# Kernel optimization log

Hardware: AMD Instinct MI355X
Metric: run time of the kernel (lower is better)

## Reference

```python
import math
import jax, jax.numpy as jnp
import numpy as np

B, L = 2, 4096
D_MODEL, D_STATE, D_CONV, EXPAND = 1024, 64, 4, 2
D_INNER = EXPAND * D_MODEL
DT_RANK = max(1, D_MODEL // 16)
EPS = float(jnp.finfo(jnp.float32).eps)  # torch nn.RMSNorm default eps


def setup_inputs() -> dict:
    key = jax.random.key(0)
    ks = jax.random.split(key, 8)
    sc = lambda k, shape, scale: jax.random.normal(k, shape, jnp.float32) * scale
    x = jax.random.normal(ks[0], (B, L, D_MODEL), jnp.float32)
    in_proj_w = sc(ks[1], (2 * D_INNER, D_MODEL), D_MODEL ** -0.5)
    conv_w = sc(ks[2], (D_INNER, 1, D_CONV), D_CONV ** -0.5)  # depthwise kernel
    conv_b = jnp.zeros((D_INNER,), jnp.float32)
    norm_w = jnp.ones((D_INNER,), jnp.float32)
    dt_std = DT_RANK ** -0.5
    dt_w = jax.random.uniform(ks[3], (D_INNER, D_INNER), jnp.float32, -dt_std, dt_std)
    dt_b = jnp.full((D_INNER,), math.log(0.5), jnp.float32)
    A_log = jnp.log(jnp.tile(jnp.arange(1, D_STATE + 1, dtype=jnp.float32), (D_INNER, 1)))
    D = jnp.ones((D_INNER,), jnp.float32)
    B_w = sc(ks[4], (D_STATE, D_INNER), D_INNER ** -0.5)
    C_w = sc(ks[5], (D_STATE, D_INNER), D_INNER ** -0.5)
    out_w = sc(ks[6], (D_MODEL, D_INNER), D_INNER ** -0.5)
    return dict(x=x, in_proj_w=in_proj_w, conv_w=conv_w, conv_b=conv_b,
                norm_w=norm_w, dt_w=dt_w, dt_b=dt_b, A_log=A_log, D=D,
                B_w=B_w, C_w=C_w, out_w=out_w)


def _mamba2_fwd(x, in_proj_w, conv_w, conv_b, norm_w, dt_w, dt_b, A_log, D, B_w, C_w, out_w):
    batch, seq_len, _ = x.shape
    # input projection + gating
    xg = x @ in_proj_w.T                               # [B, L, 2*d_inner]
    x_inner, gate = jnp.split(xg, 2, axis=-1)
    x_inner = x_inner * jax.nn.silu(gate)
    # causal depthwise conv1d (left pad d_conv-1, keep first L outputs)
    lhs = x_inner.transpose(0, 2, 1)                   # [B, d_inner, L]
    conv = jax.lax.conv_general_dilated(
        lhs, conv_w, window_strides=(1,), padding=[(D_CONV - 1, 0)],
        feature_group_count=conv_w.shape[0])
    x_conv = (conv + conv_b[None, :, None]).transpose(0, 2, 1)  # [B, L, d_inner]
    # RMSNorm
    x_conv = x_conv * jax.lax.rsqrt(jnp.mean(x_conv ** 2, axis=-1, keepdims=True) + EPS) * norm_w
    # SSM parameters
    dt = jax.nn.softplus(x_conv @ dt_w.T + dt_b)       # [B, L, d_inner]
    A = -jnp.exp(A_log)                                # [d_inner, d_state]
    Bt = x_conv @ B_w.T                                # [B, L, d_state]
    Ct = x_conv @ C_w.T                                # [B, L, d_state]

    # selective scan: h_t = exp(dt_t * A) * h_{t-1} + dt_t * B_t * x_t
    def step(h, inp):
        dt_t, b_t, c_t, xc_t = inp                     # [B,d], [B,N], [B,N], [B,d]
        A_bar = jnp.exp(dt_t[..., None] * A)           # [B, d_inner, d_state]
        h = A_bar * h + (dt_t * xc_t)[..., None] * b_t[:, None, :]
        y_t = jnp.einsum('bdn,bn->bd', h, c_t)
        return h, y_t

    h0 = jnp.zeros((batch, x_conv.shape[-1], D_STATE), x_conv.dtype)
    xs = (dt.transpose(1, 0, 2), Bt.transpose(1, 0, 2),
          Ct.transpose(1, 0, 2), x_conv.transpose(1, 0, 2))
    _, ys = jax.lax.scan(step, h0, xs)                 # ys: [L, B, d_inner]
    y = ys.transpose(1, 0, 2) + D * x_conv             # skip connection
    return y @ out_w.T                                 # [B, L, d_model]


def reference(x, in_proj_w, conv_w, conv_b, norm_w, dt_w, dt_b, A_log, D, B_w, C_w, out_w):
    return _mamba2_fwd(x, in_proj_w, conv_w, conv_b, norm_w, dt_w, dt_b, A_log, D, B_w, C_w, out_w)
```

## Files before the change

### kernel.cpp

```cpp
#include <hip/hip_runtime.h>
#include <cmath>

#define BB 2
#define LL 4096
#define DM 1024
#define DI 2048
#define NS 64
static constexpr float EPSF  = 1.1920928955078125e-07f;
static constexpr float LOG2E = 1.4426950408889634f;

typedef unsigned short u16;
typedef __attribute__((ext_vector_type(4))) unsigned short u16x4;
typedef __attribute__((ext_vector_type(8))) short bf16x8;
typedef __attribute__((ext_vector_type(4))) float f32x4;

__device__ __forceinline__ u16 f2bf(float f){
    unsigned u = __float_as_uint(f);
    return (u16)((u + 0x7fffu + ((u >> 16) & 1u)) >> 16);
}
__device__ __forceinline__ float bf2f(u16 h){ return __uint_as_float(((unsigned)h) << 16); }
__device__ __forceinline__ void gload16(const void* g, void* l){
    __builtin_amdgcn_global_load_lds((const __attribute__((address_space(1))) void*)g,
                                     (__attribute__((address_space(3))) void*)l, 16, 0, 0);
}

__global__ __launch_bounds__(256)
void cvtf2b(const float* __restrict__ in, u16* __restrict__ out, int n)
{
    int i = (blockIdx.x * 256 + threadIdx.x) * 4;
    float4 v = *(const float4*)(in + i);
    u16x4 o; o[0]=f2bf(v.x); o[1]=f2bf(v.y); o[2]=f2bf(v.z); o[3]=f2bf(v.w);
    *(u16x4*)(out + i) = o;
}

template<int MODE, int OUTBF>
__global__ __launch_bounds__(256)
void gemm_bf16(const u16* __restrict__ A, const u16* __restrict__ W,
               const float* __restrict__ bias, void* __restrict__ Cout,
               int M, int N, int K)
{
    __shared__ u16 As[128*32];
    __shared__ u16 Bs[128*32];
    __shared__ u16 Bg[(MODE==1) ? 128*32 : 8];

    const int tid  = threadIdx.x;
    const int lane = tid & 63;
    const int wave = tid >> 6;
    const int m0 = blockIdx.y * 128;
    const int n0 = blockIdx.x * 128;
    const int wr = wave >> 1, wc = wave & 1;

    f32x4 acc [4][4];
    f32x4 acc2[(MODE==1)?4:1][(MODE==1)?4:1];
    #pragma unroll
    for (int i=0;i<4;i++)
        #pragma unroll
        for (int j=0;j<4;j++)
            #pragma unroll
            for (int r=0;r<4;r++) acc[i][j][r] = 0.f;
    if (MODE==1){
        #pragma unroll
        for (int i=0;i<4;i++)
            #pragma unroll
            for (int j=0;j<4;j++)
                #pragma unroll
                for (int r=0;r<4;r++) acc2[i][j][r] = 0.f;
    }

    for (int k0 = 0; k0 < K; k0 += 32) {
        #pragma unroll
        for (int it = 0; it < 2; ++it) {
            const int s  = it*256 + tid;
            const int r  = s >> 2;
            const int q  = s & 3;
            const int qs = q ^ ((r >> 1) & 3);
            const int ub = (it*256 + wave*64) * 8;
            gload16(A + (size_t)(m0 + r)*K + k0 + qs*8, As + ub);
            gload16(W + (size_t)(n0 + r)*K + k0 + qs*8, Bs + ub);
            if (MODE==1)
                gload16(W + (size_t)(N + n0 + r)*K + k0 + qs*8, Bg + ub);
        }
        __syncthreads();

        bf16x8 af[4], bfr[4], bgr[(MODE==1)?4:1];
        #pragma unroll
        for (int mi=0; mi<4; ++mi){
            const int r  = wr*64 + mi*16 + (lane & 15);
            const int qs = (lane >> 4) ^ ((r >> 1) & 3);
            af[mi] = *(const bf16x8*)(As + (r*4 + qs)*8);
        }
        #pragma unroll
        for (int ni=0; ni<4; ++ni){
            const int c  = wc*64 + ni*16 + (lane & 15);
            const int qs = (lane >> 4) ^ ((c >> 1) & 3);
            bfr[ni] = *(const bf16x8*)(Bs + (c*4 + qs)*8);
            if (MODE==1) bgr[ni] = *(const bf16x8*)(Bg + (c*4 + qs)*8);
        }
        #pragma unroll
        for (int mi=0; mi<4; ++mi)
            #pragma unroll
            for (int ni=0; ni<4; ++ni){
                acc[mi][ni] = __builtin_amdgcn_mfma_f32_16x16x32_bf16(af[mi], bfr[ni], acc[mi][ni], 0,0,0);
                if (MODE==1)
                    acc2[mi][ni] = __builtin_amdgcn_mfma_f32_16x16x32_bf16(af[mi], bgr[ni], acc2[mi][ni], 0,0,0);
            }
        __syncthreads();
    }

    #pragma unroll
    for (int mi=0; mi<4; ++mi){
        #pragma unroll
        for (int ni=0; ni<4; ++ni){
            const int col = n0 + wc*64 + ni*16 + (lane & 15);
            #pragma unroll
            for (int rj=0; rj<4; ++rj){
                const int row = m0 + wr*64 + mi*16 + (lane >> 4)*4 + rj;
                float v = acc[mi][ni][rj];
                if (MODE==1){
                    float g = acc2[mi][ni][rj];
                    v = v * (g / (1.f + __expf(-g)));
                }
                if (MODE==2){
                    float z = v + bias[col];
                    v = (z > 20.f) ? z : log1pf(__expf(z));
                }
                if (MODE==3){
                    ((float*)Cout)[((size_t)row*64 + (col & 63))*2 + (col >> 6)] = v;
                } else if (OUTBF) {
                    ((u16*)Cout)[(size_t)row*N + col] = f2bf(v);
                } else {
                    ((float*)Cout)[(size_t)row*N + col] = v;
                }
            }
        }
    }
}

__global__ __launch_bounds__(256)
void conv_rms(const u16* __restrict__ xin, const float* __restrict__ cw,
              const float* __restrict__ cb, const float* __restrict__ nw,
              u16* __restrict__ xc)
{
    const int bl  = blockIdx.x;
    const int l   = bl & (LL-1);
    const int tid = threadIdx.x;
    const int d0  = tid * 8;

    float a[8];
    #pragma unroll
    for (int j=0;j<8;j++) a[j] = cb[d0+j];
    #pragma unroll
    for (int t=0;t<4;t++){
        const int ls = l - 3 + t;
        if (ls >= 0){
            bf16x8 xv = *(const bf16x8*)(xin + (size_t)(bl-3+t)*DI + d0);
            #pragma unroll
            for (int j=0;j<8;j++)
                a[j] += bf2f((u16)xv[j]) * cw[(d0+j)*4 + t];
        }
    }
    float ss = 0.f;
    #pragma unroll
    for (int j=0;j<8;j++) ss += a[j]*a[j];
    ss += __shfl_xor(ss,32); ss += __shfl_xor(ss,16); ss += __shfl_xor(ss,8);
    ss += __shfl_xor(ss,4);  ss += __shfl_xor(ss,2);  ss += __shfl_xor(ss,1);
    __shared__ float red[4];
    if ((tid & 63)==0) red[tid>>6] = ss;
    __syncthreads();
    const float tot   = red[0]+red[1]+red[2]+red[3];
    const float scale = rsqrtf(tot * (1.f/DI) + EPSF);
    u16x4 o0, o1;
    #pragma unroll
    for (int j=0;j<4;j++) o0[j] = f2bf(a[j]  *scale*nw[d0+j]);
    #pragma unroll
    for (int j=0;j<4;j++) o1[j] = f2bf(a[4+j]*scale*nw[d0+4+j]);
    *(u16x4*)(xc + (size_t)bl*DI + d0)     = o0;
    *(u16x4*)(xc + (size_t)bl*DI + d0 + 4) = o1;
}

__global__ __launch_bounds__(256)
void transpose_bf(const u16* __restrict__ in, u16* __restrict__ out, int R, int C)
{
    __shared__ u16 t[32][36];
    const int b  = blockIdx.z;
    const int r0 = blockIdx.y * 32;
    const int c0 = blockIdx.x * 32;
    const int ir = threadIdx.x >> 3;
    const int ic = (threadIdx.x & 7) * 4;
    const size_t base = (size_t)b * R * C;

    u16x4 v = *(const u16x4*)(in + base + (size_t)(r0+ir)*C + c0 + ic);
    #pragma unroll
    for (int k=0;k<4;k++) t[ir][ic+k] = v[k];
    __syncthreads();
    u16x4 o;
    #pragma unroll
    for (int k=0;k<4;k++) o[k] = t[ic+k][ir];
    *(u16x4*)(out + base + (size_t)(c0+ir)*R + r0 + ic) = o;
}

#define BSTAGE(MU) \
    { _Pragma("unroll") \
      for (int i=0;i<MU;i++){ \
          const bool g = (lane & MU) != 0; \
          float q = g ? p[i] : p[i+MU]; \
          float r = __shfl_xor(q, MU); \
          p[i] = (g ? p[i+MU] : p[i]) + r; \
      } }

__global__ __launch_bounds__(512)
void scan4(const u16* __restrict__ dtT, const u16* __restrict__ xcT,
           const float* __restrict__ BCi, const float* __restrict__ A_log,
           const float* __restrict__ Dp, u16* __restrict__ yT)
{
    __shared__ float lbc[2][64*128];
    __shared__ float dtu[8][64][2];
    const int tid  = threadIdx.x;
    const int lane = tid & 63;
    const int wave = tid >> 6;
    const int b    = blockIdx.x >> 8;
    const int d    = (blockIdx.x & 255) * 8 + wave;

    const float Ac = -__expf(A_log[d*NS + lane]) * LOG2E;
    const float Dd = Dp[d];
    const size_t chbase = ((size_t)b*DI + d) * LL;
    const u16* dtp = dtT + chbase;
    const u16* xcp = xcT + chbase;
    u16*       yp  = yT  + chbase;
    const float* bcb = BCi + (size_t)b * LL * 128;

    auto stage = [&](int t0, int bufi){
        const float* src = bcb + (size_t)t0 * 128;
        #pragma unroll
        for (int i=0;i<4;i++){
            const int slot = i*512 + wave*64;
            gload16(src + (size_t)(slot + lane)*4, &lbc[bufi][slot*4]);
        }
    };

    stage(0, 0);
    asm volatile("s_waitcnt vmcnt(0)" ::: "memory");
    __syncthreads();

    float h = 0.f;
    int cur = 0;
    for (int t0 = 0; t0 < LL; t0 += 64) {
        if (t0 + 64 < LL) stage(t0 + 64, cur ^ 1);

        const float dtL = bf2f(dtp[t0 + lane]);
        const float xcL = bf2f(xcp[t0 + lane]);
        *(float2*)&dtu[wave][lane][0] = make_float2(dtL, dtL * xcL);
        const float* lb = lbc[cur];
        const float* dub = &dtu[wave][0][0];

        float p[64];
        #pragma unroll
        for (int j=0;j<64;j++){
            const float2 du = *(const float2*)(dub + j*2);
            const float2 bc = *(const float2*)(lb + (j*64 + lane)*2);
            const float a   = exp2f(du.x * Ac);
            h = a*h + du.y*bc.x;
            p[j] = h * bc.y;
        }
        BSTAGE(32) BSTAGE(16) BSTAGE(8) BSTAGE(4) BSTAGE(2) BSTAGE(1)
        {
            float yv = p[0] + Dd * xcL;
            unsigned pk;
            asm("v_cvt_pk_bf16_f32 %0, %1, %2" : "=v"(pk) : "v"(yv), "v"(yv));
            yp[t0 + lane] = (u16)pk;
        }

        asm volatile("s_waitcnt vmcnt(0)" ::: "memory");
        __syncthreads();
        cur ^= 1;
    }
}

extern "C" void kernel_launch(void* const* d_in, const int* in_sizes, int n_in,
                              void* d_out, int out_size, void* d_ws, size_t ws_size,
                              hipStream_t stream) {
    const float* x       = (const float*)d_in[0];
    const float* in_proj = (const float*)d_in[1];
    const float* conv_w  = (const float*)d_in[2];
    const float* conv_b  = (const float*)d_in[3];
    const float* norm_w  = (const float*)d_in[4];
    const float* dt_w    = (const float*)d_in[5];
    const float* dt_b    = (const float*)d_in[6];
    const float* A_log   = (const float*)d_in[7];
    const float* Dp      = (const float*)d_in[8];
    const float* B_w     = (const float*)d_in[9];
    const float* C_w     = (const float*)d_in[10];
    const float* out_w   = (const float*)d_in[11];

    const int M = BB * LL;
    u16* wsu = (u16*)d_ws;
    u16*   x_bf   = wsu;
    u16*   ip_bf  = wsu + (size_t)M*DM;
    u16*   dtw_bf = ip_bf + (size_t)2*DI*DM;
    u16*   xin_bf = dtw_bf + (size_t)DI*DI;
    u16*   xc_bf  = xin_bf + (size_t)M*DI;
    float* BC     = (float*)(xc_bf + (size_t)M*DI);
    u16*   bcw_bf = (u16*)(BC + (size_t)M*128);
    u16*   ow_bf  = bcw_bf + (size_t)128*DI;
    u16*   dt_bf  = xin_bf;
    u16*   dtT_bf = x_bf;
    u16*   xcT_bf = xin_bf;
    u16*   yT_bf  = xc_bf;
    u16*   y_bf   = xin_bf;

    cvtf2b<<<(M*DM)/1024, 256, 0, stream>>>(x, x_bf, M*DM);
    cvtf2b<<<(2*DI*DM)/1024, 256, 0, stream>>>(in_proj, ip_bf, 2*DI*DM);
    cvtf2b<<<(DI*DI)/1024, 256, 0, stream>>>(dt_w, dtw_bf, DI*DI);
    cvtf2b<<<(DM*DI)/1024, 256, 0, stream>>>(out_w, ow_bf, DM*DI);
    cvtf2b<<<(NS*DI)/1024, 256, 0, stream>>>(B_w, bcw_bf, NS*DI);
    cvtf2b<<<(NS*DI)/1024, 256, 0, stream>>>(C_w, bcw_bf + (size_t)NS*DI, NS*DI);

    gemm_bf16<1,1><<<dim3(DI/128, M/128), 256, 0, stream>>>(
        x_bf, ip_bf, nullptr, xin_bf, M, DI, DM);

    conv_rms<<<M, 256, 0, stream>>>(xin_bf, conv_w, conv_b, norm_w, xc_bf);

    gemm_bf16<2,1><<<dim3(DI/128, M/128), 256, 0, stream>>>(
        xc_bf, dtw_bf, dt_b, dt_bf, M, DI, DI);

    gemm_bf16<3,0><<<dim3(1, M/128), 256, 0, stream>>>(
        xc_bf, bcw_bf, nullptr, BC, M, 128, DI);

    transpose_bf<<<dim3(DI/32, LL/32, BB), 256, 0, stream>>>(dt_bf, dtT_bf, LL, DI);
    transpose_bf<<<dim3(DI/32, LL/32, BB), 256, 0, stream>>>(xc_bf, xcT_bf, LL, DI);

    scan4<<<BB*DI/8, 512, 0, stream>>>(dtT_bf, xcT_bf, BC, A_log, Dp, yT_bf);

    transpose_bf<<<dim3(LL/32, DI/32, BB), 256, 0, stream>>>(yT_bf, y_bf, DI, LL);

    gemm_bf16<0,0><<<dim3(DM/128, M/128), 256, 0, stream>>>(
        y_bf, ow_bf, nullptr, (float*)d_out, M, DM, DI);
}
```

Before: 1.059 ms.

## Single-buffer scan LDS with register prefetch of next chunk

Replaces the double-buffered async global-to-LDS staging of B/C in the scan kernel with a single LDS buffer. The next chunk of B/C, dt and x is prefetched into registers during compute and written to LDS between two barriers. This halves LDS use (64KB to 32KB per block) and adds a min-blocks launch bound, aiming for more resident blocks and better latency hiding. The cost is extra register pressure from the prefetch and an extra barrier per chunk.

Result: slower. 1.341 ms (+26.6%).

```diff
diff --git a/kernel.cpp b/kernel.cpp
--- a/kernel.cpp
+++ b/kernel.cpp
@@ -208,12 +208,12 @@
           p[i] = (g ? p[i+MU] : p[i]) + r; \
       } }
 
-__global__ __launch_bounds__(512)
-void scan4(const u16* __restrict__ dtT, const u16* __restrict__ xcT,
+__global__ __launch_bounds__(512, 6)
+void scan5(const u16* __restrict__ dtT, const u16* __restrict__ xcT,
            const float* __restrict__ BCi, const float* __restrict__ A_log,
            const float* __restrict__ Dp, u16* __restrict__ yT)
 {
-    __shared__ float lbc[2][64*128];
+    __shared__ float lbc[64*128];
     __shared__ float dtu[8][64][2];
     const int tid  = threadIdx.x;
     const int lane = tid & 63;
@@ -229,35 +229,38 @@
     u16*       yp  = yT  + chbase;
     const float* bcb = BCi + (size_t)b * LL * 128;
 
-    auto stage = [&](int t0, int bufi){
-        const float* src = bcb + (size_t)t0 * 128;
-        #pragma unroll
-        for (int i=0;i<4;i++){
-            const int slot = i*512 + wave*64;
-            gload16(src + (size_t)(slot + lane)*4, &lbc[bufi][slot*4]);
-        }
-    };
-
-    stage(0, 0);
-    asm volatile("s_waitcnt vmcnt(0)" ::: "memory");
+    {
+        float4 br0[4];
+        #pragma unroll
+        for (int i=0;i<4;i++) br0[i] = *(const float4*)(bcb + (size_t)(tid + i*512)*4);
+        const float dt0 = bf2f(dtp[lane]);
+        const float xc0 = bf2f(xcp[lane]);
+        #pragma unroll
+        for (int i=0;i<4;i++) *(float4*)&lbc[(size_t)(tid + i*512)*4] = br0[i];
+        *(float2*)&dtu[wave][lane][0] = make_float2(dt0, dt0 * xc0);
+    }
+    float xcL = bf2f(xcp[lane]);
     __syncthreads();
 
     float h = 0.f;
-    int cur = 0;
     for (int t0 = 0; t0 < LL; t0 += 64) {
-        if (t0 + 64 < LL) stage(t0 + 64, cur ^ 1);
-
-        const float dtL = bf2f(dtp[t0 + lane]);
-        const float xcL = bf2f(xcp[t0 + lane]);
-        *(float2*)&dtu[wave][lane][0] = make_float2(dtL, dtL * xcL);
-        const float* lb = lbc[cur];
+        const bool more = (t0 + 64 < LL);
+        float4 brN[4];
+        float dtN = 0.f, xcN = 0.f;
+        if (more) {
+            const float* srcN = bcb + (size_t)(t0 + 64) * 128;
+            #pragma unroll
+            for (int i=0;i<4;i++) brN[i] = *(const float4*)(srcN + (size_t)(tid + i*512)*4);
+            dtN = bf2f(dtp[t0 + 64 + lane]);
+            xcN = bf2f(xcp[t0 + 64 + lane]);
+        }
+
         const float* dub = &dtu[wave][0][0];
-
         float p[64];
         #pragma unroll
         for (int j=0;j<64;j++){
             const float2 du = *(const float2*)(dub + j*2);
-            const float2 bc = *(const float2*)(lb + (j*64 + lane)*2);
+            const float2 bc = *(const float2*)(&lbc[(size_t)(j*64 + lane)*2]);
             const float a   = exp2f(du.x * Ac);
             h = a*h + du.y*bc.x;
             p[j] = h * bc.y;
@@ -270,9 +273,14 @@
             yp[t0 + lane] = (u16)pk;
         }
 
-        asm volatile("s_waitcnt vmcnt(0)" ::: "memory");
-        __syncthreads();
-        cur ^= 1;
+        if (more) {
+            __syncthreads();
+            #pragma unroll
+            for (int i=0;i<4;i++) *(float4*)&lbc[(size_t)(tid + i*512)*4] = brN[i];
+            *(float2*)&dtu[wave][lane][0] = make_float2(dtN, dtN * xcN);
+            __syncthreads();
+            xcL = xcN;
+        }
     }
 }
 
@@ -329,7 +337,7 @@
     transpose_bf<<<dim3(DI/32, LL/32, BB), 256, 0, stream>>>(dt_bf, dtT_bf, LL, DI);
     transpose_bf<<<dim3(DI/32, LL/32, BB), 256, 0, stream>>>(xc_bf, xcT_bf, LL, DI);
 
-    scan4<<<BB*DI/8, 512, 0, stream>>>(dtT_bf, xcT_bf, BC, A_log, Dp, yT_bf);
+    scan5<<<BB*DI/8, 512, 0, stream>>>(dtT_bf, xcT_bf, BC, A_log, Dp, yT_bf);
 
     transpose_bf<<<dim3(LL/32, DI/32, BB), 256, 0, stream>>>(yT_bf, y_bf, DI, LL);
 
```

## Fuse dt transpose into GEMM epilogue and use permlane32 swap in scan reduction

Applied to the files above, without the earlier changes.

Adds a GEMM epilogue mode that applies bias and softplus, then writes dt directly in channel-major [B, DI, L] layout as 4-element bf16 vectors. This removes one standalone transpose kernel and its extra round trip through memory. The workspace aliasing for dtT and xcT is swapped so the GEMM output does not clobber inputs that are still needed. Separately, the first butterfly stage of the scan's cross-lane reduction now uses v_permlane32_swap instead of a shuffle. The strided epilogue writes (8-byte chunks spread across channels) may coalesce poorly.

Result: faster. 985.0 us (-7.0%).

```diff
diff --git a/kernel.cpp b/kernel.cpp
--- a/kernel.cpp
+++ b/kernel.cpp
@@ -112,24 +112,38 @@
         #pragma unroll
         for (int ni=0; ni<4; ++ni){
             const int col = n0 + wc*64 + ni*16 + (lane & 15);
-            #pragma unroll
-            for (int rj=0; rj<4; ++rj){
-                const int row = m0 + wr*64 + mi*16 + (lane >> 4)*4 + rj;
-                float v = acc[mi][ni][rj];
-                if (MODE==1){
-                    float g = acc2[mi][ni][rj];
-                    v = v * (g / (1.f + __expf(-g)));
+            if (MODE==4){
+                u16x4 o;
+                #pragma unroll
+                for (int rj=0; rj<4; ++rj){
+                    float z = acc[mi][ni][rj] + bias[col];
+                    float v = (z > 20.f) ? z : log1pf(__expf(z));
+                    o[rj] = f2bf(v);
                 }
-                if (MODE==2){
-                    float z = v + bias[col];
-                    v = (z > 20.f) ? z : log1pf(__expf(z));
-                }
-                if (MODE==3){
-                    ((float*)Cout)[((size_t)row*64 + (col & 63))*2 + (col >> 6)] = v;
-                } else if (OUTBF) {
-                    ((u16*)Cout)[(size_t)row*N + col] = f2bf(v);
-                } else {
-                    ((float*)Cout)[(size_t)row*N + col] = v;
+                const int rb = m0 + wr*64 + mi*16 + (lane >> 4)*4;
+                const int bb = rb >> 12;
+                const int l  = rb & (LL-1);
+                *(u16x4*)((u16*)Cout + ((size_t)bb*DI + col)*LL + l) = o;
+            } else {
+                #pragma unroll
+                for (int rj=0; rj<4; ++rj){
+                    const int row = m0 + wr*64 + mi*16 + (lane >> 4)*4 + rj;
+                    float v = acc[mi][ni][rj];
+                    if (MODE==1){
+                        float g = acc2[mi][ni][rj];
+                        v = v * (g / (1.f + __expf(-g)));
+                    }
+                    if (MODE==2){
+                        float z = v + bias[col];
+                        v = (z > 20.f) ? z : log1pf(__expf(z));
+                    }
+                    if (MODE==3){
+                        ((float*)Cout)[((size_t)row*64 + (col & 63))*2 + (col >> 6)] = v;
+                    } else if (OUTBF) {
+                        ((u16*)Cout)[(size_t)row*N + col] = f2bf(v);
+                    } else {
+                        ((float*)Cout)[(size_t)row*N + col] = v;
+                    }
                 }
             }
         }
@@ -209,7 +223,7 @@
       } }
 
 __global__ __launch_bounds__(512)
-void scan4(const u16* __restrict__ dtT, const u16* __restrict__ xcT,
+void scan9(const u16* __restrict__ dtT, const u16* __restrict__ xcT,
            const float* __restrict__ BCi, const float* __restrict__ A_log,
            const float* __restrict__ Dp, u16* __restrict__ yT)
 {
@@ -262,7 +276,13 @@
             h = a*h + du.y*bc.x;
             p[j] = h * bc.y;
         }
-        BSTAGE(32) BSTAGE(16) BSTAGE(8) BSTAGE(4) BSTAGE(2) BSTAGE(1)
+        #pragma unroll
+        for (int i=0;i<32;i++){
+            float a0 = p[i], b0 = p[i+32];
+            asm("v_permlane32_swap_b32 %0, %1" : "+v"(a0), "+v"(b0));
+            p[i] = a0 + b0;
+        }
+        BSTAGE(16) BSTAGE(8) BSTAGE(4) BSTAGE(2) BSTAGE(1)
         {
             float yv = p[0] + Dd * xcL;
             unsigned pk;
@@ -302,9 +322,8 @@
     float* BC     = (float*)(xc_bf + (size_t)M*DI);
     u16*   bcw_bf = (u16*)(BC + (size_t)M*128);
     u16*   ow_bf  = bcw_bf + (size_t)128*DI;
-    u16*   dt_bf  = xin_bf;
-    u16*   dtT_bf = x_bf;
-    u16*   xcT_bf = xin_bf;
+    u16*   dtT_bf = xin_bf;
+    u16*   xcT_bf = x_bf;
     u16*   yT_bf  = xc_bf;
     u16*   y_bf   = xin_bf;
 
@@ -320,16 +339,15 @@
 
     conv_rms<<<M, 256, 0, stream>>>(xin_bf, conv_w, conv_b, norm_w, xc_bf);
 
-    gemm_bf16<2,1><<<dim3(DI/128, M/128), 256, 0, stream>>>(
-        xc_bf, dtw_bf, dt_b, dt_bf, M, DI, DI);
+    gemm_bf16<4,1><<<dim3(DI/128, M/128), 256, 0, stream>>>(
+        xc_bf, dtw_bf, dt_b, dtT_bf, M, DI, DI);
 
     gemm_bf16<3,0><<<dim3(1, M/128), 256, 0, stream>>>(
         xc_bf, bcw_bf, nullptr, BC, M, 128, DI);
 
-    transpose_bf<<<dim3(DI/32, LL/32, BB), 256, 0, stream>>>(dt_bf, dtT_bf, LL, DI);
     transpose_bf<<<dim3(DI/32, LL/32, BB), 256, 0, stream>>>(xc_bf, xcT_bf, LL, DI);
 
-    scan4<<<BB*DI/8, 512, 0, stream>>>(dtT_bf, xcT_bf, BC, A_log, Dp, yT_bf);
+    scan9<<<BB*DI/8, 512, 0, stream>>>(dtT_bf, xcT_bf, BC, A_log, Dp, yT_bf);
 
     transpose_bf<<<dim3(LL/32, DI/32, BB), 256, 0, stream>>>(yT_bf, y_bf, DI, LL);
 
```
